# Kernel tuning notes

Measured on AMD Instinct MI355X. Metric: run time of the kernel, lower is better.

Reference implementation:

```python
import jax, jax.numpy as jnp
import numpy as np

N_HEADS = 16
N_KV_HEADS = 8
N_REP = 2
HEAD_DIM = 128
SOFTCAP = 50.0
NEG_INF = -2.3819763e38
ROPE_BASE = 10000.0


def _rotate_half(x):
    x1, x2 = jnp.split(x, 2, axis=-1)
    return jnp.concatenate((-x2, x1), axis=-1)


def _rope_cos_sin(seq_len, dtype):
    # Gemma2RotaryEmbedding: inv_freq over even dims, emb = cat(freqs, freqs)
    inv_freq = 1.0 / (ROPE_BASE ** (jnp.arange(0, HEAD_DIM, 2, dtype=jnp.float32) / HEAD_DIM))
    freqs = jnp.arange(seq_len, dtype=jnp.float32)[:, None] * inv_freq[None, :]  # [s, hd/2]
    emb = jnp.concatenate((freqs, freqs), axis=-1)  # [s, hd]
    return jnp.cos(emb).astype(dtype), jnp.sin(emb).astype(dtype)


def setup_inputs() -> dict:
    key = jax.random.key(0)
    ks = jax.random.split(key, 5)
    b, s, d = 2, 2048, 2048
    w_scale = 0.02
    return {
        "x": jax.random.normal(ks[0], (b, s, d), dtype=jnp.float32),
        "wq": jax.random.normal(ks[1], (N_HEADS * HEAD_DIM, d), dtype=jnp.float32) * w_scale,
        "wk": jax.random.normal(ks[2], (N_KV_HEADS * HEAD_DIM, d), dtype=jnp.float32) * w_scale,
        "wv": jax.random.normal(ks[3], (N_KV_HEADS * HEAD_DIM, d), dtype=jnp.float32) * w_scale,
        "wo": jax.random.normal(ks[4], (d, N_HEADS * HEAD_DIM), dtype=jnp.float32) * w_scale,
    }


def reference(x, wq, wk, wv, wo):
    b, s, d = x.shape
    # QKV projections (linear_fn = plain x @ W.T)
    xq = (x @ wq.T).reshape(b, s, N_HEADS, HEAD_DIM).transpose(0, 2, 1, 3)      # [b,h,s,hd]
    xk = (x @ wk.T).reshape(b, s, N_KV_HEADS, HEAD_DIM).transpose(0, 2, 1, 3)   # [b,kv,s,hd]
    xv = (x @ wv.T).reshape(b, s, N_KV_HEADS, HEAD_DIM).transpose(0, 2, 1, 3)
    # Gemma2 rotary on q, k
    cos, sin = _rope_cos_sin(s, x.dtype)  # [s,hd] each, broadcast over b,h
    xq = xq * cos + _rotate_half(xq) * sin
    xk = xk * cos + _rotate_half(xk) * sin
    # repeat_kv: expand kv heads to n_heads
    keys = jnp.repeat(xk, N_REP, axis=1)
    values = jnp.repeat(xv, N_REP, axis=1)
    # scores with scaling and Gemma2 logit softcapping
    scale = float(HEAD_DIM) ** -0.5
    scores = jnp.einsum("bhsd,bhtd->bhst", xq * scale, keys)
    scores = jnp.tanh(scores / SOFTCAP) * SOFTCAP
    # causal additive mask [s, t]
    q_pos = jnp.arange(s)[:, None]
    k_pos = jnp.arange(s)[None, :]
    mask = jnp.where(k_pos <= q_pos, 0.0, NEG_INF).astype(jnp.float32)
    scores = scores + mask  # broadcast over [b,h]
    probs = jax.nn.softmax(scores.astype(jnp.float32), axis=-1).astype(xq.dtype)
    out = jnp.einsum("bhst,bhtd->bhsd", probs, values)
    out = out.transpose(0, 2, 1, 3).reshape(b, s, N_HEADS * HEAD_DIM)
    return out @ wo.T
```

## Files before the change

kernel.cpp:

```cpp
#include <hip/hip_runtime.h>
#include <stdint.h>
#include <stddef.h>

#define S_LEN   2048
#define DMODEL  2048
#define NHEADS  16
#define NKVH    8
#define HD      128
#define QPRE 1.7677669529663688e-3f
#define C1 72.13475204444817f

typedef __attribute__((ext_vector_type(8))) short  short8;
typedef __attribute__((ext_vector_type(4))) float  float4v;

static __device__ __forceinline__ unsigned short f2bf(float f) {
  union { float f; unsigned int u; } v; v.f = f;
  unsigned int u = v.u;
  u += 0x7fffu + ((u >> 16) & 1u);
  return (unsigned short)(u >> 16);
}
static __device__ __forceinline__ float bf2f(unsigned short b) {
  union { unsigned int u; float f; } v; v.u = ((unsigned int)b) << 16;
  return v.f;
}
static __device__ __forceinline__ void gload_lds16(const void* g, void* l) {
  __builtin_amdgcn_global_load_lds(
      (const __attribute__((address_space(1))) void*)g,
      (__attribute__((address_space(3))) void*)l, 16, 0, 0);
}

__global__ __launch_bounds__(256) void cvt_all(
    const float* __restrict__ x,  const float* __restrict__ wq,
    const float* __restrict__ wk, const float* __restrict__ wv,
    const float* __restrict__ wo,
    ushort4* __restrict__ xb, ushort4* __restrict__ wcat,
    ushort4* __restrict__ wob) {
  int i = blockIdx.x * 256 + threadIdx.x;
  const float4* src; ushort4* dst; int j;
  if (i < 2097152)      { src = (const float4*)x;  dst = xb;             j = i; }
  else if (i < 3145728) { src = (const float4*)wq; dst = wcat;           j = i - 2097152; }
  else if (i < 3670016) { src = (const float4*)wk; dst = wcat + 1048576; j = i - 3145728; }
  else if (i < 4194304) { src = (const float4*)wv; dst = wcat + 1572864; j = i - 3670016; }
  else                  { src = (const float4*)wo; dst = wob;            j = i - 4194304; }
  float4 v = src[j];
  ushort4 o;
  o.x = f2bf(v.x); o.y = f2bf(v.y); o.z = f2bf(v.z); o.w = f2bf(v.w);
  dst[j] = o;
}

__global__ __launch_bounds__(512, 2) void gemm256_qkv(
    const unsigned short* __restrict__ A,
    const unsigned short* __restrict__ B,
    unsigned short* __restrict__ C) {
  const int t    = threadIdx.x;
  const int lane = t & 63;
  const int w    = t >> 6;
  const int l15  = lane & 15;
  const int quad = lane >> 4;

  const int id  = blockIdx.x;
  const int swz = (id & 7) * 32 + (id >> 3);
  const int m0  = (swz >> 4) * 256;
  const int n0  = (swz & 15) * 256;

  __shared__ unsigned short sm[2][2][2][128 * 64];

  const int wm  = w >> 2;
  const int wnq = w & 3;
  const int hB  = wnq >> 1;
  const int wnl = (wnq & 1) * 64;

  int soff[2];
#pragma unroll
  for (int i = 0; i < 2; ++i) {
    int P = (w * 2 + i) * 64 + lane;
    int r = P >> 3;
    int lc = (P & 7) ^ (r & 7);
    soff[i] = r * DMODEL + lc * 8;
  }
  const unsigned short* Ab = A + (size_t)m0 * DMODEL;
  const unsigned short* Bb = B + (size_t)n0 * DMODEL;

  auto stage = [&](int mat, int half, int buf, int kt) {
    const unsigned short* g =
        (mat ? Bb : Ab) + (size_t)half * 128 * DMODEL + kt * 64;
    unsigned short* l = &sm[buf][mat][half][(w * 2) * 512];
#pragma unroll
    for (int i = 0; i < 2; ++i)
      gload_lds16(g + soff[i], l + i * 512);
  };

  float4v acc[2][2][4][2];
#pragma unroll
  for (int qm = 0; qm < 2; ++qm)
#pragma unroll
    for (int qn = 0; qn < 2; ++qn)
#pragma unroll
      for (int mt = 0; mt < 4; ++mt)
#pragma unroll
        for (int nt = 0; nt < 2; ++nt)
          acc[qm][qn][mt][nt] = (float4v){0.f, 0.f, 0.f, 0.f};

  stage(0, 0, 0, 0); stage(0, 1, 0, 0); stage(1, 0, 0, 0); stage(1, 1, 0, 0);
  stage(0, 0, 1, 1); stage(0, 1, 1, 1); stage(1, 0, 1, 1);
  asm volatile("s_waitcnt vmcnt(6)" ::: "memory");
  __builtin_amdgcn_s_barrier();

  const int NT = DMODEL / 64;
#pragma unroll 1
  for (int j = 0; j < NT; ++j) {
    const int c = j & 1;
    const unsigned short* As = &sm[c][0][wm][0];
    const unsigned short* Bs = &sm[c][1][hB][0];
    short8 af[4][2], ag[4][2], bf0[2][2], bf1[2][2];

    if (j + 1 < NT) stage(1, 1, c ^ 1, j + 1);

#pragma unroll
    for (int mt = 0; mt < 4; ++mt)
#pragma unroll
      for (int kk = 0; kk < 2; ++kk) {
        int r = mt * 16 + l15;
        af[mt][kk] = *(const short8*)&As[r * 64 + (((kk * 4 + quad) ^ (r & 7)) * 8)];
      }
#pragma unroll
    for (int nt = 0; nt < 2; ++nt)
#pragma unroll
      for (int kk = 0; kk < 2; ++kk) {
        int r = wnl + nt * 16 + l15;
        bf0[nt][kk] = *(const short8*)&Bs[r * 64 + (((kk * 4 + quad) ^ (r & 7)) * 8)];
      }
    __builtin_amdgcn_s_setprio(1);
#pragma unroll
    for (int mt = 0; mt < 4; ++mt)
#pragma unroll
      for (int nt = 0; nt < 2; ++nt)
#pragma unroll
        for (int kk = 0; kk < 2; ++kk)
          acc[0][0][mt][nt] = __builtin_amdgcn_mfma_f32_16x16x32_bf16(
              af[mt][kk], bf0[nt][kk], acc[0][0][mt][nt], 0, 0, 0);
    __builtin_amdgcn_s_setprio(0);

#pragma unroll
    for (int nt = 0; nt < 2; ++nt)
#pragma unroll
      for (int kk = 0; kk < 2; ++kk) {
        int r = wnl + 32 + nt * 16 + l15;
        bf1[nt][kk] = *(const short8*)&Bs[r * 64 + (((kk * 4 + quad) ^ (r & 7)) * 8)];
      }
    __builtin_amdgcn_s_setprio(1);
#pragma unroll
    for (int mt = 0; mt < 4; ++mt)
#pragma unroll
      for (int nt = 0; nt < 2; ++nt)
#pragma unroll
        for (int kk = 0; kk < 2; ++kk)
          acc[0][1][mt][nt] = __builtin_amdgcn_mfma_f32_16x16x32_bf16(
              af[mt][kk], bf1[nt][kk], acc[0][1][mt][nt], 0, 0, 0);
    __builtin_amdgcn_s_setprio(0);

#pragma unroll
    for (int mt = 0; mt < 4; ++mt)
#pragma unroll
      for (int kk = 0; kk < 2; ++kk) {
        int r = 64 + mt * 16 + l15;
        ag[mt][kk] = *(const short8*)&As[r * 64 + (((kk * 4 + quad) ^ (r & 7)) * 8)];
      }
    asm volatile("s_waitcnt lgkmcnt(0)" ::: "memory");
    __builtin_amdgcn_s_barrier();
    if (j + 2 < NT) {
      stage(0, 0, c, j + 2); stage(0, 1, c, j + 2); stage(1, 0, c, j + 2);
    }
    __builtin_amdgcn_s_setprio(1);
#pragma unroll
    for (int mt = 0; mt < 4; ++mt)
#pragma unroll
      for (int nt = 0; nt < 2; ++nt)
#pragma unroll
        for (int kk = 0; kk < 2; ++kk)
          acc[1][0][mt][nt] = __builtin_amdgcn_mfma_f32_16x16x32_bf16(
              ag[mt][kk], bf0[nt][kk], acc[1][0][mt][nt], 0, 0, 0);
#pragma unroll
    for (int mt = 0; mt < 4; ++mt)
#pragma unroll
      for (int nt = 0; nt < 2; ++nt)
#pragma unroll
        for (int kk = 0; kk < 2; ++kk)
          acc[1][1][mt][nt] = __builtin_amdgcn_mfma_f32_16x16x32_bf16(
              ag[mt][kk], bf1[nt][kk], acc[1][1][mt][nt], 0, 0, 0);
    __builtin_amdgcn_s_setprio(0);
    if (j + 2 < NT)      { asm volatile("s_waitcnt vmcnt(6)" ::: "memory"); }
    else if (j + 1 < NT) { asm volatile("s_waitcnt vmcnt(0)" ::: "memory"); }
    __builtin_amdgcn_s_barrier();
  }

#pragma unroll
  for (int qm = 0; qm < 2; ++qm)
#pragma unroll
    for (int mt = 0; mt < 4; ++mt) {
      int row0 = m0 + wm * 128 + qm * 64 + mt * 16 + quad * 4;
      int b = row0 >> 11, s0 = row0 & (S_LEN - 1);
#pragma unroll
      for (int qn = 0; qn < 2; ++qn)
#pragma unroll
        for (int nt = 0; nt < 2; ++nt) {
          int col = n0 + wnq * 64 + qn * 32 + nt * 16 + l15;
          float4v v = acc[qm][qn][mt][nt];
          if (col < 2048) {
            int head = col >> 7, d = col & (HD - 1);
#pragma unroll
            for (int r2 = 0; r2 < 4; ++r2)
              C[((size_t)(b * 16 + head) * S_LEN + s0 + r2) * HD + d] = f2bf(v[r2]);
          } else if (col < 3072) {
            int c2 = col - 2048;
            int kvh = c2 >> 7, d = c2 & (HD - 1);
#pragma unroll
            for (int r2 = 0; r2 < 4; ++r2)
              C[8388608 + ((size_t)(b * 8 + kvh) * S_LEN + s0 + r2) * HD + d] = f2bf(v[r2]);
          } else {
            int c2 = col - 3072;
            int kvh = c2 >> 7, d = c2 & (HD - 1);
            ushort4 pk;
            pk.x = f2bf(v[0]); pk.y = f2bf(v[1]);
            pk.z = f2bf(v[2]); pk.w = f2bf(v[3]);
            *(ushort4*)&C[12582912 + ((size_t)(b * 8 + kvh) * HD + d) * S_LEN + s0] = pk;
          }
        }
    }
}

__global__ __launch_bounds__(512, 2) void gemm256_out(
    const unsigned short* __restrict__ A,
    const unsigned short* __restrict__ B,
    float* __restrict__ C) {
  const int t    = threadIdx.x;
  const int lane = t & 63;
  const int w    = t >> 6;
  const int l15  = lane & 15;
  const int quad = lane >> 4;

  const int id  = blockIdx.x;
  const int swz = (id & 7) * 32 + (id >> 3);
  const int m0  = (swz >> 4) * 256;
  const int n0  = (swz & 15) * 128;

  __shared__ unsigned short sm[2][3][128 * 64];

  const int wm = w >> 1;
  const int wn = w & 1;
  const int hA = wm >> 1;
  const int ra0 = (wm & 1) * 64;

  int soff[2];
#pragma unroll
  for (int i = 0; i < 2; ++i) {
    int P = (w * 2 + i) * 64 + lane;
    int r = P >> 3;
    int lc = (P & 7) ^ (r & 7);
    soff[i] = r * DMODEL + lc * 8;
  }
  const unsigned short* Ab = A + (size_t)m0 * DMODEL;
  const unsigned short* Bb = B + (size_t)n0 * DMODEL;

  auto stage = [&](int region, int buf, int kt) {
    const unsigned short* g =
        (region == 2 ? Bb : Ab + (size_t)region * 128 * DMODEL) + kt * 64;
    unsigned short* l = &sm[buf][region][(w * 2) * 512];
#pragma unroll
    for (int i = 0; i < 2; ++i)
      gload_lds16(g + soff[i], l + i * 512);
  };

  float4v acc[4][4];
#pragma unroll
  for (int mt = 0; mt < 4; ++mt)
#pragma unroll
    for (int nt = 0; nt < 4; ++nt)
      acc[mt][nt] = (float4v){0.f, 0.f, 0.f, 0.f};

  stage(0, 0, 0); stage(1, 0, 0); stage(2, 0, 0);
  stage(0, 1, 1); stage(1, 1, 1); stage(2, 1, 1);
  asm volatile("s_waitcnt vmcnt(6)" ::: "memory");
  __builtin_amdgcn_s_barrier();

  const int NT = DMODEL / 64;
#pragma unroll 1
  for (int j = 0; j < NT; ++j) {
    const int c = j & 1;
    const unsigned short* As = &sm[c][hA][0];
    const unsigned short* Bs = &sm[c][2][0];
    short8 af[4][2], bf[4][2];

#pragma unroll
    for (int mt = 0; mt < 4; ++mt)
#pragma unroll
      for (int kk = 0; kk < 2; ++kk) {
        int r = ra0 + mt * 16 + l15;
        af[mt][kk] = *(const short8*)&As[r * 64 + (((kk * 4 + quad) ^ (r & 7)) * 8)];
      }
#pragma unroll
    for (int nt = 0; nt < 4; ++nt)
#pragma unroll
      for (int kk = 0; kk < 2; ++kk) {
        int r = wn * 64 + nt * 16 + l15;
        bf[nt][kk] = *(const short8*)&Bs[r * 64 + (((kk * 4 + quad) ^ (r & 7)) * 8)];
      }
    asm volatile("s_waitcnt lgkmcnt(0)" ::: "memory");
    __builtin_amdgcn_s_barrier();
    if (j + 2 < NT) { stage(0, c, j + 2); stage(1, c, j + 2); stage(2, c, j + 2); }

    __builtin_amdgcn_s_setprio(1);
#pragma unroll
    for (int mt = 0; mt < 4; ++mt)
#pragma unroll
      for (int nt = 0; nt < 4; ++nt)
#pragma unroll
        for (int kk = 0; kk < 2; ++kk)
          acc[mt][nt] = __builtin_amdgcn_mfma_f32_16x16x32_bf16(
              af[mt][kk], bf[nt][kk], acc[mt][nt], 0, 0, 0);
    __builtin_amdgcn_s_setprio(0);

    if (j + 2 < NT)      { asm volatile("s_waitcnt vmcnt(6)" ::: "memory"); }
    else if (j + 1 < NT) { asm volatile("s_waitcnt vmcnt(0)" ::: "memory"); }
    __builtin_amdgcn_s_barrier();
  }

#pragma unroll
  for (int mt = 0; mt < 4; ++mt) {
    int row = m0 + wm * 64 + mt * 16 + quad * 4;
#pragma unroll
    for (int nt = 0; nt < 4; ++nt) {
      int col = n0 + wn * 64 + nt * 16 + l15;
#pragma unroll
      for (int r2 = 0; r2 < 4; ++r2)
        C[(size_t)(row + r2) * 2048 + col] = acc[mt][nt][r2];
    }
  }
}

__global__ __launch_bounds__(256) void rope_kernel(unsigned short* __restrict__ Q,
                                                   unsigned short* __restrict__ Kc) {
  int gt = blockIdx.x * 256 + threadIdx.x;
  int r = gt >> 6;
  int j = gt & 63;
  const int QROWS = 2 * NHEADS * S_LEN;
  bool isQ = (r < QROWS);
  unsigned short* p = isQ ? (Q + (size_t)r * HD)
                          : (Kc + (size_t)(r - QROWS) * HD);
  int pos = r & (S_LEN - 1);
  float inv = exp2f(-(float)j * 0.20762050593046868f);
  float ang = (float)pos * inv;
  float c = cosf(ang), s = sinf(ang);
  float sc = isQ ? QPRE : 1.0f;
  float x1 = bf2f(p[j]), x2 = bf2f(p[j + 64]);
  p[j]      = f2bf((x1 * c - x2 * s) * sc);
  p[j + 64] = f2bf((x2 * c + x1 * s) * sc);
}

__global__ __launch_bounds__(256, 2) void attn_kernel(
    const unsigned short* __restrict__ Q,
    const unsigned short* __restrict__ Kc,
    const unsigned short* __restrict__ Vt,
    unsigned short* __restrict__ Aout) {
  const int t    = threadIdx.x;
  const int lane = t & 63;
  const int w    = t >> 6;
  const int l15  = lane & 15;
  const int quad = lane >> 4;
  const int bh = blockIdx.x;
  const int pp = blockIdx.y;
  const int b = bh >> 4, h = bh & 15, kv = h >> 1;
  const int qtA = pp, qtB = 31 - pp;
  const int q0A = qtA * 64, q0B = qtB * 64;
  const int ntB = qtB + 1;

  __shared__ unsigned short Kt[64 * 128];
  __shared__ unsigned short Vts[128 * 64];
  __shared__ unsigned short Pt[4 * 2 * 1024];

  int offK[4], offV[4];
#pragma unroll
  for (int i = 0; i < 4; ++i) {
    int g = i * 256 + t;
    int rK = g >> 4, cK = (g & 15) ^ (rK & 7);
    offK[i] = rK * HD + cK * 8;
    int rV = g >> 3, cV = (g & 7) ^ (rV & 7);
    offV[i] = rV * S_LEN + cV * 8;
  }

  const unsigned short* QA = Q + ((size_t)(b * NHEADS + h) * S_LEN + q0A + w * 16) * HD;
  const unsigned short* QB = Q + ((size_t)(b * NHEADS + h) * S_LEN + q0B + w * 16) * HD;
  short8 qfA[4], qfB[4];
#pragma unroll
  for (int kk = 0; kk < 4; ++kk) {
    qfA[kk] = *(const short8*)&QA[l15 * HD + kk * 32 + quad * 8];
    qfB[kk] = *(const short8*)&QB[l15 * HD + kk * 32 + quad * 8];
  }

  float4v oA[8], oB[8];
#pragma unroll
  for (int nth = 0; nth < 8; ++nth) {
    oA[nth] = (float4v){0.f, 0.f, 0.f, 0.f};
    oB[nth] = (float4v){0.f, 0.f, 0.f, 0.f};
  }
  float lsA = 0.f, lsB = 0.f;

  const unsigned short* kg0 = Kc + (size_t)(b * NKVH + kv) * S_LEN * HD;
  const unsigned short* vg0 = Vt + (size_t)(b * NKVH + kv) * HD * S_LEN;
  unsigned short* PB = Pt + (w * 2 + 0) * 1024;
  unsigned short* PA = Pt + (w * 2 + 1) * 1024;

  auto stage = [&](int kt) {
    const unsigned short* kgp = kg0 + (size_t)kt * 64 * HD;
    const unsigned short* vgp = vg0 + (size_t)kt * 64;
#pragma unroll
    for (int i = 0; i < 4; ++i)
      gload_lds16(kgp + offK[i], &Kt[(i * 256 + w * 64) * 8]);
#pragma unroll
    for (int i = 0; i < 4; ++i)
      gload_lds16(vgp + offV[i], &Vts[(i * 256 + w * 64) * 8]);
  };

  auto softcap = [&](float x) -> float {
    float xx = __builtin_amdgcn_fmed3f(x, -0.26f, 0.26f);
    float x2 = xx * xx;
    float u = __builtin_fmaf(0.13333334f, x2, -0.33333334f);
    float v = __builtin_fmaf(u, x2, 1.0f);
    return __builtin_amdgcn_exp2f((C1 * xx) * v);
  };

  stage(0);
  for (int kt = 0; kt < ntB; ++kt) {
    __syncthreads();
    const bool doA   = (kt <= qtA);
    const bool diagA = (kt == qtA);
    const bool diagB = (kt == qtB);
    const unsigned short* Kb = Kt;
    const unsigned short* Vb = Vts;

#pragma unroll
    for (int ntk = 0; ntk < 4; ++ntk) {
      int pb = l15 * 64 + (((ntk * 2 + (quad >> 1)) ^ (l15 & 7)) * 8) + (quad & 1) * 4;
      short8 kf[4];
#pragma unroll
      for (int kk = 0; kk < 4; ++kk)
        kf[kk] = *(const short8*)
            &Kb[(ntk * 16 + l15) * HD + (((kk * 4 + quad) ^ (l15 & 7)) * 8)];

      if (diagB && (ntk * 16 > w * 16 + 15)) {
        uint2 z; z.x = 0u; z.y = 0u;
        *(uint2*)&PB[pb] = z;
      } else {
        float4v s0 = (float4v){0.f, 0.f, 0.f, 0.f};
#pragma unroll
        for (int kk = 0; kk < 4; ++kk)
          s0 = __builtin_amdgcn_mfma_f32_16x16x32_bf16(kf[kk], qfB[kk], s0, 0, 0, 0);
        float pv[4];
#pragma unroll
        for (int r = 0; r < 4; ++r) {
          float p = softcap(s0[r]);
          if (diagB)
            p = (ntk * 16 + quad * 4 + r <= w * 16 + l15) ? p : 0.f;
          lsB += p;
          pv[r] = p;
        }
        union { float f; unsigned u; } u0, u1, u2, u3;
        u0.f = pv[0]; u1.f = pv[1]; u2.f = pv[2]; u3.f = pv[3];
        uint2 pk;
        pk.x = __builtin_amdgcn_perm(u1.u, u0.u, 0x07060302);
        pk.y = __builtin_amdgcn_perm(u3.u, u2.u, 0x07060302);
        *(uint2*)&PB[pb] = pk;
      }

      if (doA) {
        if (diagA && (ntk * 16 > w * 16 + 15)) {
          uint2 z; z.x = 0u; z.y = 0u;
          *(uint2*)&PA[pb] = z;
        } else {
          float4v s0 = (float4v){0.f, 0.f, 0.f, 0.f};
#pragma unroll
          for (int kk = 0; kk < 4; ++kk)
            s0 = __builtin_amdgcn_mfma_f32_16x16x32_bf16(kf[kk], qfA[kk], s0, 0, 0, 0);
          float pv[4];
#pragma unroll
          for (int r = 0; r < 4; ++r) {
            float p = softcap(s0[r]);
            if (diagA)
              p = (ntk * 16 + quad * 4 + r <= w * 16 + l15) ? p : 0.f;
            lsA += p;
            pv[r] = p;
          }
          union { float f; unsigned u; } u0, u1, u2, u3;
          u0.f = pv[0]; u1.f = pv[1]; u2.f = pv[2]; u3.f = pv[3];
          uint2 pk;
          pk.x = __builtin_amdgcn_perm(u1.u, u0.u, 0x07060302);
          pk.y = __builtin_amdgcn_perm(u3.u, u2.u, 0x07060302);
          *(uint2*)&PA[pb] = pk;
        }
      }
    }

#pragma unroll
    for (int kk = 0; kk < 2; ++kk) {
      int sw = ((kk * 4 + quad) ^ (l15 & 7)) * 8;
      short8 pB0 = *(const short8*)&PB[l15 * 64 + sw];
      short8 pA0;
      if (doA) pA0 = *(const short8*)&PA[l15 * 64 + sw];
#pragma unroll
      for (int nth = 0; nth < 8; ++nth) {
        short8 vf = *(const short8*)&Vb[(nth * 16 + l15) * 64 + sw];
        oB[nth] = __builtin_amdgcn_mfma_f32_16x16x32_bf16(pB0, vf, oB[nth], 0, 0, 0);
        if (doA)
          oA[nth] = __builtin_amdgcn_mfma_f32_16x16x32_bf16(pA0, vf, oA[nth], 0, 0, 0);
      }
    }
    __syncthreads();
    if (kt + 1 < ntB) stage(kt + 1);
  }

#pragma unroll
  for (int tile = 0; tile < 2; ++tile) {
    float ls = tile ? lsA : lsB;
    float4v* oo = tile ? oA : oB;
    int q0 = tile ? q0A : q0B;
    float v = ls;
    v += __shfl_xor(v, 16, 64);
    v += __shfl_xor(v, 32, 64);
    float inv = __builtin_amdgcn_rcpf(v);
    float iv[4];
#pragma unroll
    for (int r = 0; r < 4; ++r) iv[r] = __shfl(inv, quad * 4 + r, 64);
    unsigned short* ob = Aout + (size_t)(b * S_LEN + q0 + w * 16) * DMODEL + h * HD;
#pragma unroll
    for (int nth = 0; nth < 8; ++nth) {
#pragma unroll
      for (int r = 0; r < 4; ++r) {
        int row = quad * 4 + r;
        ob[(size_t)row * DMODEL + nth * 16 + l15] = f2bf(oo[nth][r] * iv[r]);
      }
    }
  }
}

extern "C" void kernel_launch(void* const* d_in, const int* in_sizes, int n_in,
                              void* d_out, int out_size, void* d_ws, size_t ws_size,
                              hipStream_t stream) {
  const float* x  = (const float*)d_in[0];
  const float* wq = (const float*)d_in[1];
  const float* wk = (const float*)d_in[2];
  const float* wv = (const float*)d_in[3];
  const float* wo = (const float*)d_in[4];

  char* ws = (char*)d_ws;
  unsigned short* xb   = (unsigned short*)(ws + 0);
  unsigned short* wcat = (unsigned short*)(ws + 16777216);
  unsigned short* wob  = (unsigned short*)(ws + 33554432);
  unsigned short* QKV  = (unsigned short*)(ws + 41943040);
  unsigned short* AO   = (unsigned short*)(ws + 75497472);

  unsigned short* Qw = QKV;
  unsigned short* Kw = QKV + 8388608;
  unsigned short* Vw = QKV + 12582912;

  cvt_all<<<20480, 256, 0, stream>>>(x, wq, wk, wv, wo,
                                     (ushort4*)xb, (ushort4*)wcat, (ushort4*)wob);

  gemm256_qkv<<<256, 512, 0, stream>>>(xb, wcat, QKV);

  rope_kernel<<<24576, 256, 0, stream>>>(Qw, Kw);

  attn_kernel<<<dim3(32, 16), 256, 0, stream>>>(Qw, Kw, Vw, AO);

  gemm256_out<<<256, 512, 0, stream>>>(AO, wob, (float*)d_out);
}
```

Baseline: 306.7 us.

## Keep softmax probabilities in registers and feed PV MFMA directly, skipping LDS round-trip

The score tile P is no longer written to and reread from shared memory. The S accumulator layout is reused directly as the B operand of a 16x16x16 bf16 MFMA with V as the A operand, so the output is computed transposed. Fully masked diagonal sub-tiles are now skipped instead of being zero-filled. The output store becomes vectorized 4-element writes per lane with no shuffles. This trades one 16x16x32 MFMA for two 16x16x16 MFMAs per tile and changes the access pattern of the V loads from LDS.

New measurement: 333.6 us. 8.8% more time.

```diff
diff --git a/kernel.cpp b/kernel.cpp
--- a/kernel.cpp
+++ b/kernel.cpp
@@ -11,6 +11,7 @@
 #define C1 72.13475204444817f
 
 typedef __attribute__((ext_vector_type(8))) short  short8;
+typedef __attribute__((ext_vector_type(4))) short  short4v;
 typedef __attribute__((ext_vector_type(4))) float  float4v;
 
 static __device__ __forceinline__ unsigned short f2bf(float f) {
@@ -376,7 +377,6 @@
 
   __shared__ unsigned short Kt[64 * 128];
   __shared__ unsigned short Vts[128 * 64];
-  __shared__ unsigned short Pt[4 * 2 * 1024];
 
   int offK[4], offV[4];
 #pragma unroll
@@ -407,8 +407,6 @@
 
   const unsigned short* kg0 = Kc + (size_t)(b * NKVH + kv) * S_LEN * HD;
   const unsigned short* vg0 = Vt + (size_t)(b * NKVH + kv) * HD * S_LEN;
-  unsigned short* PB = Pt + (w * 2 + 0) * 1024;
-  unsigned short* PA = Pt + (w * 2 + 1) * 1024;
 
   auto stage = [&](int kt) {
     const unsigned short* kgp = kg0 + (size_t)kt * 64 * HD;
@@ -435,22 +433,21 @@
     const bool doA   = (kt <= qtA);
     const bool diagA = (kt == qtA);
     const bool diagB = (kt == qtB);
-    const unsigned short* Kb = Kt;
-    const unsigned short* Vb = Vts;
 
 #pragma unroll
     for (int ntk = 0; ntk < 4; ++ntk) {
-      int pb = l15 * 64 + (((ntk * 2 + (quad >> 1)) ^ (l15 & 7)) * 8) + (quad & 1) * 4;
+      const bool mB = !(diagB && (ntk * 16 > w * 16 + 15));
+      const bool mA = doA && !(diagA && (ntk * 16 > w * 16 + 15));
+      if (!(mB || mA)) continue;
+
       short8 kf[4];
 #pragma unroll
       for (int kk = 0; kk < 4; ++kk)
         kf[kk] = *(const short8*)
-            &Kb[(ntk * 16 + l15) * HD + (((kk * 4 + quad) ^ (l15 & 7)) * 8)];
-
-      if (diagB && (ntk * 16 > w * 16 + 15)) {
-        uint2 z; z.x = 0u; z.y = 0u;
-        *(uint2*)&PB[pb] = z;
-      } else {
+            &Kt[(ntk * 16 + l15) * HD + (((kk * 4 + quad) ^ (l15 & 7)) * 8)];
+
+      short4v pB, pA;
+      if (mB) {
         float4v s0 = (float4v){0.f, 0.f, 0.f, 0.f};
 #pragma unroll
         for (int kk = 0; kk < 4; ++kk)
@@ -466,54 +463,46 @@
         }
         union { float f; unsigned u; } u0, u1, u2, u3;
         u0.f = pv[0]; u1.f = pv[1]; u2.f = pv[2]; u3.f = pv[3];
-        uint2 pk;
-        pk.x = __builtin_amdgcn_perm(u1.u, u0.u, 0x07060302);
-        pk.y = __builtin_amdgcn_perm(u3.u, u2.u, 0x07060302);
-        *(uint2*)&PB[pb] = pk;
-      }
-
-      if (doA) {
-        if (diagA && (ntk * 16 > w * 16 + 15)) {
-          uint2 z; z.x = 0u; z.y = 0u;
-          *(uint2*)&PA[pb] = z;
-        } else {
-          float4v s0 = (float4v){0.f, 0.f, 0.f, 0.f};
-#pragma unroll
-          for (int kk = 0; kk < 4; ++kk)
-            s0 = __builtin_amdgcn_mfma_f32_16x16x32_bf16(kf[kk], qfA[kk], s0, 0, 0, 0);
-          float pv[4];
-#pragma unroll
-          for (int r = 0; r < 4; ++r) {
-            float p = softcap(s0[r]);
-            if (diagA)
-              p = (ntk * 16 + quad * 4 + r <= w * 16 + l15) ? p : 0.f;
-            lsA += p;
-            pv[r] = p;
-          }
-          union { float f; unsigned u; } u0, u1, u2, u3;
-          u0.f = pv[0]; u1.f = pv[1]; u2.f = pv[2]; u3.f = pv[3];
-          uint2 pk;
-          pk.x = __builtin_amdgcn_perm(u1.u, u0.u, 0x07060302);
-          pk.y = __builtin_amdgcn_perm(u3.u, u2.u, 0x07060302);
-          *(uint2*)&PA[pb] = pk;
+        union { unsigned u[2]; short4v s; } pk;
+        pk.u[0] = __builtin_amdgcn_perm(u1.u, u0.u, 0x07060302);
+        pk.u[1] = __builtin_amdgcn_perm(u3.u, u2.u, 0x07060302);
+        pB = pk.s;
+      }
+      if (mA) {
+        float4v s0 = (float4v){0.f, 0.f, 0.f, 0.f};
+#pragma unroll
+        for (int kk = 0; kk < 4; ++kk)
+          s0 = __builtin_amdgcn_mfma_f32_16x16x32_bf16(kf[kk], qfA[kk], s0, 0, 0, 0);
+        float pv[4];
+#pragma unroll
+        for (int r = 0; r < 4; ++r) {
+          float p = softcap(s0[r]);
+          if (diagA)
+            p = (ntk * 16 + quad * 4 + r <= w * 16 + l15) ? p : 0.f;
+          lsA += p;
+          pv[r] = p;
         }
+        union { float f; unsigned u; } u0, u1, u2, u3;
+        u0.f = pv[0]; u1.f = pv[1]; u2.f = pv[2]; u3.f = pv[3];
+        union { unsigned u[2]; short4v s; } pk;
+        pk.u[0] = __builtin_amdgcn_perm(u1.u, u0.u, 0x07060302);
+        pk.u[1] = __builtin_amdgcn_perm(u3.u, u2.u, 0x07060302);
+        pA = pk.s;
+      }
+
+#pragma unroll
+      for (int nth = 0; nth < 8; ++nth) {
+        int row = nth * 16 + l15;
+        int caddr = row * 64 + (((ntk * 2 + (quad >> 1)) ^ (l15 & 7)) * 8)
+                    + (quad & 1) * 4;
+        short4v vf = *(const short4v*)&Vts[caddr];
+        if (mB)
+          oB[nth] = __builtin_amdgcn_mfma_f32_16x16x16bf16_1k(vf, pB, oB[nth], 0, 0, 0);
+        if (mA)
+          oA[nth] = __builtin_amdgcn_mfma_f32_16x16x16bf16_1k(vf, pA, oA[nth], 0, 0, 0);
       }
     }
 
-#pragma unroll
-    for (int kk = 0; kk < 2; ++kk) {
-      int sw = ((kk * 4 + quad) ^ (l15 & 7)) * 8;
-      short8 pB0 = *(const short8*)&PB[l15 * 64 + sw];
-      short8 pA0;
-      if (doA) pA0 = *(const short8*)&PA[l15 * 64 + sw];
-#pragma unroll
-      for (int nth = 0; nth < 8; ++nth) {
-        short8 vf = *(const short8*)&Vb[(nth * 16 + l15) * 64 + sw];
-        oB[nth] = __builtin_amdgcn_mfma_f32_16x16x32_bf16(pB0, vf, oB[nth], 0, 0, 0);
-        if (doA)
-          oA[nth] = __builtin_amdgcn_mfma_f32_16x16x32_bf16(pA0, vf, oA[nth], 0, 0, 0);
-      }
-    }
     __syncthreads();
     if (kt + 1 < ntB) stage(kt + 1);
   }
@@ -527,17 +516,16 @@
     v += __shfl_xor(v, 16, 64);
     v += __shfl_xor(v, 32, 64);
     float inv = __builtin_amdgcn_rcpf(v);
-    float iv[4];
-#pragma unroll
-    for (int r = 0; r < 4; ++r) iv[r] = __shfl(inv, quad * 4 + r, 64);
-    unsigned short* ob = Aout + (size_t)(b * S_LEN + q0 + w * 16) * DMODEL + h * HD;
+    unsigned short* ob = Aout + (size_t)(b * S_LEN + q0 + w * 16 + l15) * DMODEL
+                         + h * HD + quad * 4;
 #pragma unroll
     for (int nth = 0; nth < 8; ++nth) {
-#pragma unroll
-      for (int r = 0; r < 4; ++r) {
-        int row = quad * 4 + r;
-        ob[(size_t)row * DMODEL + nth * 16 + l15] = f2bf(oo[nth][r] * iv[r]);
-      }
+      ushort4 st;
+      st.x = f2bf(oo[nth][0] * inv);
+      st.y = f2bf(oo[nth][1] * inv);
+      st.z = f2bf(oo[nth][2] * inv);
+      st.w = f2bf(oo[nth][3] * inv);
+      *(ushort4*)&ob[nth * 16] = st;
     }
   }
 }
```
